# Performance work log

Hardware: AMD Instinct MI355X
Metric: run time of the kernel (lower is better)

The kernel has to match this reference:

```python
import jax, jax.numpy as jnp
import numpy as np

N_COLS = 107
CAT_SLICES = [(1, 10), (10, 26), (27, 34), (34, 49), (49, 55), (55, 60), (60, 62), (65, 107)]
MSE_COLS = [0, 26, 62, 63, 64]
BATCH = 524288


def setup_inputs() -> dict:
    key = jax.random.key(0)
    k_dec, k_cont, k_cat = jax.random.split(key, 3)
    data_decoded = jax.random.normal(k_dec, (BATCH, N_COLS), dtype=jnp.float32)
    # Build data_true: continuous cols random, categorical slices exactly one-hot.
    data_true = jax.random.uniform(k_cont, (BATCH, N_COLS), dtype=jnp.float32)
    rows = jnp.arange(BATCH)
    for i, (s, e) in enumerate(CAT_SLICES):
        kk = jax.random.fold_in(k_cat, i)
        labels = jax.random.randint(kk, (BATCH,), 0, e - s)
        data_true = data_true.at[:, s:e].set(0.0)
        data_true = data_true.at[rows, s + labels].set(1.0)
    return {"data_decoded": data_decoded, "data_true": data_true, "batch_size": BATCH}


def _ce(logits, onehot_true):
    # torch nonzero()[:,1] on an exact one-hot slice == argmax
    labels = jnp.argmax(onehot_true, axis=1)
    logp = jax.nn.log_softmax(logits, axis=1)
    return -jnp.mean(jnp.take_along_axis(logp, labels[:, None], axis=1))


def _mse(a, b):
    d = a - b
    return jnp.mean(d * d)


def reference(data_decoded, data_true, batch_size):
    mse_loss = jnp.float32(0.0)
    for c in MSE_COLS:
        mse_loss = mse_loss + _mse(data_decoded[:, c], data_true[:, c])
    ce_loss = jnp.float32(0.0)
    for s, e in CAT_SLICES:
        ce_loss = ce_loss + _ce(data_decoded[:, s:e], data_true[:, s:e])
    multi_loss = mse_loss + ce_loss
    return multi_loss, mse_loss, ce_loss
```

## Files before the change

### kernel.cpp

```cpp
#include <hip/hip_runtime.h>

#define NCOLS 107
#define ROWS_PER_TILE 16
#define TILE_FLOATS (ROWS_PER_TILE * NCOLS)
#define TILE_VEC (TILE_FLOATS / 4)
#define THREADS 256
#define WAVES_PER_BLOCK 4
#define BLOCKS 2048
#define TILES_PER_WAVE 4

typedef float f4 __attribute__((ext_vector_type(4)));

template<int S, int E>
__device__ __forceinline__ float slice_lse(const float* dr) {
    constexpr int L = E - S;
    float s = 0.0f;
#pragma unroll
    for (int j = 0; j < L; ++j) s += __expf(dr[S + j]);
    return __logf(s);
}

__global__ __launch_bounds__(THREADS) void multiloss_main(
        const float* __restrict__ dec, const float* __restrict__ tru,
        float2* __restrict__ ws, int ntiles) {
    __shared__ float sdec[WAVES_PER_BLOCK * TILE_FLOATS];
    int gwave = (blockIdx.x * THREADS + threadIdx.x) >> 6;
    int lane  = threadIdx.x & 63;
    float* buf = sdec + (threadIdx.x >> 6) * TILE_FLOATS;

    float mse = 0.0f, dot = 0.0f, lse = 0.0f;

    for (int t = 0; t < TILES_PER_WAVE; ++t) {
        int tile = gwave * TILES_PER_WAVE + t;
        if (tile >= ntiles) break;
        const f4* gd = (const f4*)(dec + (size_t)tile * TILE_FLOATS);
        const f4* gt = (const f4*)(tru + (size_t)tile * TILE_FLOATS);

#pragma unroll
        for (int i = 0; i < 7; ++i) {
            int idx = i * 64 + lane;
            if (idx < TILE_VEC) {
                f4 dv = gd[idx];
                f4 tv = gt[idx];
                ((f4*)buf)[idx] = dv;
                int col0 = (idx * 4) % NCOLS;
#pragma unroll
                for (int k = 0; k < 4; ++k) {
                    int col = col0 + k;
                    if (col >= NCOLS) col -= NCOLS;
                    float d = dv[k], tt = tv[k];
                    bool ismse = (col == 0) | (col == 26) |
                                 ((unsigned)(col - 62) <= 2u);
                    float df = d - tt;
                    mse += ismse ? df * df : 0.0f;
                    dot += ismse ? 0.0f : d * tt;
                }
            }
        }

        int row  = lane & 15;
        int part = lane >> 4;
        const float* dr = buf + row * NCOLS;
        if (part == 0) {
            lse += slice_lse<65, 107>(dr);
        } else if (part == 1) {
            lse += slice_lse<10, 26>(dr) + slice_lse<34, 49>(dr);
        } else if (part == 2) {
            lse += slice_lse<1, 10>(dr) + slice_lse<27, 34>(dr)
                 + slice_lse<49, 55>(dr);
        } else {
            lse += slice_lse<55, 60>(dr) + slice_lse<60, 62>(dr);
        }
    }

    float ce = lse - dot;
#pragma unroll
    for (int off = 32; off > 0; off >>= 1) {
        mse += __shfl_down(mse, off, 64);
        ce  += __shfl_down(ce,  off, 64);
    }
    if (lane == 0)
        ws[gwave] = make_float2(mse, ce);
}

__global__ __launch_bounds__(256) void multiloss_fin(
        const float2* __restrict__ ws, float* __restrict__ out,
        int nslots, float invN) {
    float m = 0.0f, c = 0.0f;
    for (int i = threadIdx.x; i < nslots; i += 256) {
        float2 v = ws[i];
        m += v.x; c += v.y;
    }
#pragma unroll
    for (int off = 32; off > 0; off >>= 1) {
        m += __shfl_down(m, off, 64);
        c += __shfl_down(c, off, 64);
    }
    __shared__ float sm[4], sc[4];
    int wid  = threadIdx.x >> 6;
    int lane = threadIdx.x & 63;
    if (lane == 0) { sm[wid] = m; sc[wid] = c; }
    __syncthreads();
    if (threadIdx.x == 0) {
        float mse = (sm[0] + sm[1] + sm[2] + sm[3]) * invN;
        float ce  = (sc[0] + sc[1] + sc[2] + sc[3]) * invN;
        out[0] = mse + ce;
        out[1] = mse;
        out[2] = ce;
    }
}

extern "C" void kernel_launch(void* const* d_in, const int* in_sizes, int n_in,
                              void* d_out, int out_size, void* d_ws, size_t ws_size,
                              hipStream_t stream) {
    const float* dec = (const float*)d_in[0];
    const float* tru = (const float*)d_in[1];
    int nrows  = in_sizes[0] / NCOLS;
    int ntiles = nrows / ROWS_PER_TILE;
    int nslots = BLOCKS * THREADS / 64;
    float2* ws = (float2*)d_ws;
    multiloss_main<<<BLOCKS, THREADS, 0, stream>>>(dec, tru, ws, ntiles);
    multiloss_fin<<<1, 256, 0, stream>>>(ws, (float*)d_out, nslots,
                                         1.0f / (float)nrows);
}
```

Before: 448.1 us.

## Accumulate per-row slice exp sums via LDS atomics instead of staging tile

Stops staging each decoded tile in shared memory and running an unbalanced per-row slice LSE pass afterwards. Each lane now computes exp of its own elements while streaming and atomically adds them into per-row, per-slice bucket sums in LDS. The log of each bucket is then taken by two lanes. This spreads the exp work evenly across lanes and shrinks LDS use, but it adds four LDS float atomics per vector load, and neighbouring lanes often hit the same bucket, so those atomics can serialize.

```diff
diff --git a/kernel.cpp b/kernel.cpp
--- a/kernel.cpp
+++ b/kernel.cpp
@@ -8,25 +8,17 @@
 #define WAVES_PER_BLOCK 4
 #define BLOCKS 2048
 #define TILES_PER_WAVE 4
+#define NBUCK (ROWS_PER_TILE * 8)
 
 typedef float f4 __attribute__((ext_vector_type(4)));
-
-template<int S, int E>
-__device__ __forceinline__ float slice_lse(const float* dr) {
-    constexpr int L = E - S;
-    float s = 0.0f;
-#pragma unroll
-    for (int j = 0; j < L; ++j) s += __expf(dr[S + j]);
-    return __logf(s);
-}
 
 __global__ __launch_bounds__(THREADS) void multiloss_main(
         const float* __restrict__ dec, const float* __restrict__ tru,
         float2* __restrict__ ws, int ntiles) {
-    __shared__ float sdec[WAVES_PER_BLOCK * TILE_FLOATS];
-    int gwave = (blockIdx.x * THREADS + threadIdx.x) >> 6;
-    int lane  = threadIdx.x & 63;
-    float* buf = sdec + (threadIdx.x >> 6) * TILE_FLOATS;
+    __shared__ float sbuck[WAVES_PER_BLOCK * NBUCK];
+    int lane   = threadIdx.x & 63;
+    float* buck = sbuck + (threadIdx.x >> 6) * NBUCK;
+    int gwave  = (blockIdx.x * THREADS + threadIdx.x) >> 6;
 
     float mse = 0.0f, dot = 0.0f, lse = 0.0f;
 
@@ -36,41 +28,39 @@
         const f4* gd = (const f4*)(dec + (size_t)tile * TILE_FLOATS);
         const f4* gt = (const f4*)(tru + (size_t)tile * TILE_FLOATS);
 
+        buck[lane]      = 0.0f;
+        buck[lane + 64] = 0.0f;
+
 #pragma unroll
         for (int i = 0; i < 7; ++i) {
             int idx = i * 64 + lane;
             if (idx < TILE_VEC) {
                 f4 dv = gd[idx];
                 f4 tv = gt[idx];
-                ((f4*)buf)[idx] = dv;
-                int col0 = (idx * 4) % NCOLS;
+                unsigned c4  = (unsigned)(idx * 4);
+                unsigned row = c4 / NCOLS;
+                unsigned col = c4 - row * NCOLS;
 #pragma unroll
                 for (int k = 0; k < 4; ++k) {
-                    int col = col0 + k;
-                    if (col >= NCOLS) col -= NCOLS;
                     float d = dv[k], tt = tv[k];
                     bool ismse = (col == 0) | (col == 26) |
                                  ((unsigned)(col - 62) <= 2u);
                     float df = d - tt;
                     mse += ismse ? df * df : 0.0f;
                     dot += ismse ? 0.0f : d * tt;
+                    float e = ismse ? 0.0f : __expf(d);
+                    unsigned s = (col >= 10) + (col >= 27) + (col >= 34) +
+                                 (col >= 49) + (col >= 55) + (col >= 60) +
+                                 (col >= 65);
+                    atomicAdd(&buck[row * 8 + s], e);
+                    ++col;
+                    if (col >= NCOLS) { col = 0; ++row; }
                 }
             }
         }
-
-        int row  = lane & 15;
-        int part = lane >> 4;
-        const float* dr = buf + row * NCOLS;
-        if (part == 0) {
-            lse += slice_lse<65, 107>(dr);
-        } else if (part == 1) {
-            lse += slice_lse<10, 26>(dr) + slice_lse<34, 49>(dr);
-        } else if (part == 2) {
-            lse += slice_lse<1, 10>(dr) + slice_lse<27, 34>(dr)
-                 + slice_lse<49, 55>(dr);
-        } else {
-            lse += slice_lse<55, 60>(dr) + slice_lse<60, 62>(dr);
-        }
+        float s0 = buck[lane];
+        float s1 = buck[lane + 64];
+        lse += __logf(s0) + __logf(s1);
     }
 
     float ce = lse - dot;
```

After: 653.8 us. 45.9% more time.

## Prefetch next tile into registers in a persistent grid-stride loop

Applied to the files above, without the earlier changes.

Replaces the fixed four-tiles-per-wave loop with a persistent grid-stride loop over 1280 blocks. The next tile's decoded and true vectors are loaded into registers while the current tile's linear terms and log-sum-exp terms are computed. The partial seventh vector load now uses a clamped index with a validity mask instead of a branch, and the column index is computed incrementally. This is meant to overlap global-memory latency with compute. The cost is more live registers per thread and some load imbalance, since 5120 waves do not divide the tile count evenly.

```diff
diff --git a/kernel.cpp b/kernel.cpp
--- a/kernel.cpp
+++ b/kernel.cpp
@@ -6,8 +6,8 @@
 #define TILE_VEC (TILE_FLOATS / 4)
 #define THREADS 256
 #define WAVES_PER_BLOCK 4
-#define BLOCKS 2048
-#define TILES_PER_WAVE 4
+#define BLOCKS 1280
+#define NWAVES (BLOCKS * WAVES_PER_BLOCK)
 
 typedef float f4 __attribute__((ext_vector_type(4)));
 
@@ -20,56 +20,81 @@
     return __logf(s);
 }
 
+__device__ __forceinline__ void lin4(int idx, f4 dv, f4 tv, bool valid,
+                                     float& mse, float& dot) {
+    unsigned c4  = (unsigned)idx * 4u;
+    unsigned row = c4 / NCOLS;
+    unsigned col = c4 - row * NCOLS;
+#pragma unroll
+    for (int k = 0; k < 4; ++k) {
+        float d = dv[k], tt = tv[k];
+        bool ismse = (col == 0) | (col == 26) | ((unsigned)(col - 62) <= 2u);
+        float df = d - tt;
+        mse += (valid && ismse)  ? df * df : 0.0f;
+        dot += (valid && !ismse) ? d * tt  : 0.0f;
+        ++col; if (col >= NCOLS) col = 0;
+    }
+}
+
 __global__ __launch_bounds__(THREADS) void multiloss_main(
         const float* __restrict__ dec, const float* __restrict__ tru,
         float2* __restrict__ ws, int ntiles) {
     __shared__ float sdec[WAVES_PER_BLOCK * TILE_FLOATS];
-    int gwave = (blockIdx.x * THREADS + threadIdx.x) >> 6;
     int lane  = threadIdx.x & 63;
     float* buf = sdec + (threadIdx.x >> 6) * TILE_FLOATS;
+    f4* b4 = (f4*)buf;
+    int gwave = (blockIdx.x * THREADS + threadIdx.x) >> 6;
+
+    bool v6 = lane < (TILE_VEC - 384);
+    int  i6 = v6 ? (384 + lane) : (TILE_VEC - 1);
 
     float mse = 0.0f, dot = 0.0f, lse = 0.0f;
 
-    for (int t = 0; t < TILES_PER_WAVE; ++t) {
-        int tile = gwave * TILES_PER_WAVE + t;
-        if (tile >= ntiles) break;
-        const f4* gd = (const f4*)(dec + (size_t)tile * TILE_FLOATS);
-        const f4* gt = (const f4*)(tru + (size_t)tile * TILE_FLOATS);
+    int tile = gwave;
+    {
+        const f4* gd = (const f4*)dec + (size_t)tile * TILE_VEC;
+        const f4* gt = (const f4*)tru + (size_t)tile * TILE_VEC;
+        f4 d0 = gd[lane], d1 = gd[64+lane], d2 = gd[128+lane], d3 = gd[192+lane],
+           d4 = gd[256+lane], d5 = gd[320+lane], d6 = gd[i6];
+        f4 t0 = gt[lane], t1 = gt[64+lane], t2 = gt[128+lane], t3 = gt[192+lane],
+           t4 = gt[256+lane], t5 = gt[320+lane], t6 = gt[i6];
 
-#pragma unroll
-        for (int i = 0; i < 7; ++i) {
-            int idx = i * 64 + lane;
-            if (idx < TILE_VEC) {
-                f4 dv = gd[idx];
-                f4 tv = gt[idx];
-                ((f4*)buf)[idx] = dv;
-                int col0 = (idx * 4) % NCOLS;
-#pragma unroll
-                for (int k = 0; k < 4; ++k) {
-                    int col = col0 + k;
-                    if (col >= NCOLS) col -= NCOLS;
-                    float d = dv[k], tt = tv[k];
-                    bool ismse = (col == 0) | (col == 26) |
-                                 ((unsigned)(col - 62) <= 2u);
-                    float df = d - tt;
-                    mse += ismse ? df * df : 0.0f;
-                    dot += ismse ? 0.0f : d * tt;
-                }
+        while (tile < ntiles) {
+            b4[lane] = d0; b4[64+lane] = d1; b4[128+lane] = d2;
+            b4[192+lane] = d3; b4[256+lane] = d4; b4[320+lane] = d5;
+            b4[i6] = d6;
+            lin4(lane,     d0, t0, true, mse, dot);
+            lin4(64+lane,  d1, t1, true, mse, dot);
+            lin4(128+lane, d2, t2, true, mse, dot);
+            lin4(192+lane, d3, t3, true, mse, dot);
+            lin4(256+lane, d4, t4, true, mse, dot);
+            lin4(320+lane, d5, t5, true, mse, dot);
+            lin4(i6,       d6, t6, v6,   mse, dot);
+            int nt = tile + NWAVES;
+            if (nt < ntiles) {
+                const f4* ngd = (const f4*)dec + (size_t)nt * TILE_VEC;
+                const f4* ngt = (const f4*)tru + (size_t)nt * TILE_VEC;
+                d0 = ngd[lane]; d1 = ngd[64+lane]; d2 = ngd[128+lane];
+                d3 = ngd[192+lane]; d4 = ngd[256+lane]; d5 = ngd[320+lane];
+                d6 = ngd[i6];
+                t0 = ngt[lane]; t1 = ngt[64+lane]; t2 = ngt[128+lane];
+                t3 = ngt[192+lane]; t4 = ngt[256+lane]; t5 = ngt[320+lane];
+                t6 = ngt[i6];
             }
-        }
-
-        int row  = lane & 15;
-        int part = lane >> 4;
-        const float* dr = buf + row * NCOLS;
-        if (part == 0) {
-            lse += slice_lse<65, 107>(dr);
-        } else if (part == 1) {
-            lse += slice_lse<10, 26>(dr) + slice_lse<34, 49>(dr);
-        } else if (part == 2) {
-            lse += slice_lse<1, 10>(dr) + slice_lse<27, 34>(dr)
-                 + slice_lse<49, 55>(dr);
-        } else {
-            lse += slice_lse<55, 60>(dr) + slice_lse<60, 62>(dr);
+            int row  = lane & 15;
+            int part = lane >> 4;
+            const float* dr = buf + row * NCOLS;
+            if (part == 0) {
+                lse += slice_lse<65, 107>(dr);
+            } else if (part == 1) {
+                lse += slice_lse<10, 26>(dr) + slice_lse<34, 49>(dr);
+            } else if (part == 2) {
+                lse += slice_lse<1, 10>(dr) + slice_lse<27, 34>(dr)
+                     + slice_lse<49, 55>(dr);
+            } else {
+                lse += slice_lse<55, 60>(dr) + slice_lse<60, 62>(dr);
+            }
+            tile = nt;
         }
     }
 
@@ -117,9 +142,8 @@
     const float* tru = (const float*)d_in[1];
     int nrows  = in_sizes[0] / NCOLS;
     int ntiles = nrows / ROWS_PER_TILE;
-    int nslots = BLOCKS * THREADS / 64;
     float2* ws = (float2*)d_ws;
     multiloss_main<<<BLOCKS, THREADS, 0, stream>>>(dec, tru, ws, ntiles);
-    multiloss_fin<<<1, 256, 0, stream>>>(ws, (float*)d_out, nslots,
+    multiloss_fin<<<1, 256, 0, stream>>>(ws, (float*)d_out, NWAVES,
                                          1.0f / (float)nrows);
 }
```

After: 440.2 us. Within noise of the previous version (-1.8%).
